# Kernel optimization log

Hardware: AMD Instinct MI355X
Metric: run time of the kernel (lower is better)

Reference implementation:

```python
import jax, jax.numpy as jnp
import numpy as np
from jax import lax

D3 = 48      # manifold_dim * 3
M = 512      # mem_slots
H = 256      # slot_dim
K = 32       # topk
IN = 1024    # input_dim
ODE_HID = 128
ODE_STEPS = 2
ODE_DT = 0.5
TEMP = 1.0   # temperature buffer
LN_EPS = 1e-5


def _ln(x, g, b):
    m = jnp.mean(x, axis=-1, keepdims=True)
    v = jnp.mean(jnp.square(x - m), axis=-1, keepdims=True)
    return (x - m) * lax.rsqrt(v + LN_EPS) * g + b


def setup_inputs() -> dict:
    key = jax.random.key(0)
    ks = jax.random.split(key, 12)
    s_in = 1.0 / np.sqrt(IN)
    s_h = 1.0 / np.sqrt(H)
    s_d3 = 1.0 / np.sqrt(D3)
    s_ode = 1.0 / np.sqrt(ODE_HID)
    return {
        "x": jax.random.normal(ks[0], (16, 2048, IN), jnp.float32),
        "w1": jax.random.uniform(ks[1], (IN, D3), jnp.float32, -s_in, s_in),
        "b1": jnp.zeros((D3,), jnp.float32),
        "g1": jnp.ones((D3,), jnp.float32),
        "be1": jnp.zeros((D3,), jnp.float32),
        "wa": jax.random.uniform(ks[2], (D3, ODE_HID), jnp.float32, -s_d3, s_d3),
        "ba": jnp.zeros((ODE_HID,), jnp.float32),
        "wb": jax.random.uniform(ks[3], (ODE_HID, D3), jnp.float32, -s_ode, s_ode),
        "bb": jnp.zeros((D3,), jnp.float32),
        "mem": jax.random.normal(ks[4], (M, H), jnp.float32),
        "pos": jax.random.normal(ks[5], (M, 16, 3), jnp.float32),
        "curv": jax.random.normal(ks[6], (M, 16), jnp.float32),
        "alpha": jnp.float32(0.1),
        "wo": jax.random.uniform(ks[7], (H, IN), jnp.float32, -s_h, s_h),
        "bo": jnp.zeros((IN,), jnp.float32),
        "go": jnp.ones((IN,), jnp.float32),
        "beo": jnp.zeros((IN,), jnp.float32),
    }


def reference(x, w1, b1, g1, be1, wa, ba, wb, bb, mem, pos, curv, alpha, wo, bo, go, beo):
    # manifold projection: Linear -> LayerNorm -> GELU, viewed as (B,S,D,3)
    h = jax.nn.gelu(_ln(x @ w1 + b1, g1, be1), approximate=False)  # (B,S,48)
    # ODE evolution (2 fixed steps over the flattened manifold coords)
    for _ in range(ODE_STEPS):
        dx = jnp.tanh(h @ wa + ba) @ wb + bb
        h = h + ODE_DT * dx
    # attend: query side is detached in the original
    q = lax.stop_gradient(h)                       # (B,S,48)
    mem_pos = pos.reshape(M, -1)                   # (512,48)
    # squared pairwise L2: ||q||^2 - 2 q.m + ||m||^2
    dist = (jnp.sum(q * q, axis=-1, keepdims=True)
            - 2.0 * jnp.einsum('bsd,md->bsm', q, mem_pos)
            + jnp.sum(mem_pos * mem_pos, axis=-1))
    dist = jnp.maximum(dist, 0.0) / max(TEMP, 1e-6)
    curv_w = jnp.exp(-alpha * jnp.linalg.norm(curv, axis=-1))  # (512,)
    dist = dist * curv_w[None, None, :]
    # topk smallest distances
    neg_top, itop = lax.top_k(-dist, K)            # (B,S,K)
    w = jax.nn.softmax(neg_top, axis=-1)           # softmax(-dtop)
    slots = mem[itop]                              # (B,S,K,256) gather
    attended = jnp.einsum('bsk,bskh->bsh', w, slots)
    # output projection: Linear -> LayerNorm -> GELU
    return jax.nn.gelu(_ln(attended @ wo + bo, go, beo), approximate=False)
```

## Files before the change

kernel.cpp:

```cpp
#include <hip/hip_runtime.h>
#include <stdint.h>

typedef unsigned short u16;
typedef __attribute__((ext_vector_type(4))) short short4v;
typedef __attribute__((ext_vector_type(8))) short short8v;
typedef __attribute__((ext_vector_type(4))) float f32x4;
typedef __attribute__((address_space(1))) void gv;
typedef __attribute__((address_space(3))) void lv;

#define NTOK 32768

__device__ __forceinline__ float bf2f(u16 u){ return __uint_as_float(((uint32_t)u)<<16); }
__device__ __forceinline__ u16 f2bf(float f){
  uint32_t u = __float_as_uint(f);
  u += 0x7FFFu + ((u>>16)&1u);
  return (u16)(u>>16);
}
__device__ __forceinline__ void hilo(float v, u16& h, u16& l){
  h = f2bf(v);
  l = f2bf(v - bf2f(h));
}
__device__ __forceinline__ void tsplit(float v, u16& h, u16& l){
  uint32_t b = __float_as_uint(v);
  h = (u16)(b >> 16);
  float lf = v - __uint_as_float(b & 0xFFFF0000u);
  l = (u16)(__float_as_uint(lf) >> 16);
}
__device__ __forceinline__ void tpack8(float4 a, float4 b, short8v& hi, short8v& lo){
  float v[8] = {a.x,a.y,a.z,a.w,b.x,b.y,b.z,b.w};
  #pragma unroll
  for (int i=0;i<8;++i){ u16 h,l; tsplit(v[i],h,l); hi[i]=(short)h; lo[i]=(short)l; }
}
__device__ __forceinline__ float fexp2(float x){ float r; asm("v_exp_f32 %0, %1" : "=v"(r) : "v"(x)); return r; }
__device__ __forceinline__ float frcp(float x){ float r; asm("v_rcp_f32 %0, %1" : "=v"(r) : "v"(x)); return r; }

__device__ __forceinline__ float gelu_f(float v){ return 0.5f*v*(1.0f + erff(v*0.70710678118654752440f)); }
__device__ __forceinline__ float gelu_t(float x){
  float p = x*(2.3022141f + 0.1029435f*x*x);
  float e = fexp2(p);
  float r = frcp(e + 1.0f);
  return x*(1.0f - r);
}
__device__ __forceinline__ float tanh_f(float x){
  float e = fexp2(2.8853901f*x);
  float r = frcp(e + 1.0f);
  return 1.0f - 2.0f*r;
}

__global__ __launch_bounds__(256) void k_prep(
    const float* __restrict__ w1, const float* __restrict__ wa, const float* __restrict__ wb,
    const float* __restrict__ pos, const float* __restrict__ curv,
    const float* __restrict__ mem, const float* __restrict__ wo,
    const float* __restrict__ alpha,
    u16* __restrict__ w1s, u16* __restrict__ wah, u16* __restrict__ wbh,
    float2* __restrict__ mnw,
    u16* __restrict__ memb, u16* __restrict__ woB, u16* __restrict__ posB)
{
  int i = blockIdx.x*256 + threadIdx.x;
  if (i < 49152){ int n = i>>10, k = i&1023; u16 h,l; hilo(w1[k*48+n], h, l);
                  w1s[i] = h; w1s[49152+i] = l; return; }
  i -= 49152;
  if (i < 8192){ int u = i>>6, d = i&63; float v = (d<48) ? wa[d*128+u] : 0.f;
                 u16 h,l; hilo(v,h,l); wah[i] = h; wah[8192+i] = l; return; }
  i -= 8192;
  if (i < 6144){ int n = i>>7, u = i&127; u16 h,l; hilo(wb[u*48+n], h, l);
                 wbh[i] = h; wbh[6144+i] = l; return; }
  i -= 6144;
  if (i < 512){
    float s = 0.f;
    #pragma unroll
    for (int d=0; d<48; ++d){ float v = pos[i*48+d]; s += v*v; }
    float c2 = 0.f;
    #pragma unroll
    for (int d=0; d<16; ++d){ float v = curv[i*16+d]; c2 += v*v; }
    mnw[i] = make_float2(s, expf(-alpha[0]*sqrtf(c2)));
    return;
  }
  i -= 512;
  if (i < 131072){ memb[i] = f2bf(mem[i]); return; }
  i -= 131072;
  if (i < 262144){
    int e = i & 7, ln = (i>>3)&63, n = (i>>9)&15, cpq = (i>>13)&3, kt = i>>15;
    int col = cpq*256 + n*16 + (ln & 15);
    int k   = kt*32 + (ln >> 4)*8 + e;
    woB[i] = f2bf(wo[k*1024 + col]);
    return;
  }
  i -= 262144;
  if (i < 32768){
    int e = i & 7, ln = (i>>3)&63, n = (i>>9)&31, ks = i>>14;
    int slot = n*16 + (ln&15);
    int d = ks*32 + (ln>>4)*8 + e;
    float v = (d < 48) ? pos[slot*48 + d] : 0.f;
    u16 h,l; hilo(v,h,l);
    posB[i] = h; posB[32768+i] = l;
  }
}

__global__ __launch_bounds__(256, 2) void k_proj_ode(
    const float* __restrict__ x, const u16* __restrict__ w1s,
    const float* __restrict__ b1, const float* __restrict__ g1, const float* __restrict__ be1,
    const u16* __restrict__ wah, const u16* __restrict__ wbh,
    const float* __restrict__ ba, const float* __restrict__ bb,
    float* __restrict__ hout, float* __restrict__ q2b)
{
  extern __shared__ char dynp[];
  float* xsl = (float*)dynp;
  u16*   bsl = (u16*)(dynp + 49152);
  u16* t_hi = (u16*)dynp;
  u16* t_lo = (u16*)(dynp + 16384);
  u16* h_hi = (u16*)(dynp + 32768);
  u16* h_lo = (u16*)(dynp + 40960);

  const int tid = threadIdx.x;
  const int lane = tid & 63, w = tid >> 6;
  const int l15 = lane & 15, l4 = lane >> 4;
  const int bm = blockIdx.x;
  const int arow = w*16 + l15;
  const int kb = bm & 15;

  f32x4 acc[3];
  #pragma unroll
  for (int n=0; n<3; ++n) acc[n] = (f32x4){0.f,0.f,0.f,0.f};

  auto stage_x = [&](float* dst, int kt){
    #pragma unroll
    for (int j=0; j<4; ++j){
      int idx = (j*4 + w)*64 + lane;
      int row = idx >> 4, q = idx & 15;
      int chunk = q >> 1, half = q & 1;
      const float* src = x + (size_t)(bm*64 + row)*1024 + kt*64 + ((chunk ^ (row & 7))*8 + half*4);
      __builtin_amdgcn_global_load_lds((gv*)src, (lv*)(dst + (j*4 + w)*256), 16, 0, 0);
    }
  };
  auto stage_b = [&](u16* dst, int kt){
    #pragma unroll
    for (int j=0; j<3; ++j){
      int idx = (j*4 + w)*64 + lane;
      int hl = (idx >= 384) ? 1 : 0;
      int rr = idx - hl*384;
      int row = rr >> 3, ch = rr & 7;
      const u16* src = w1s + hl*49152 + (size_t)row*1024 + kt*64 + ((ch ^ (row & 7))*8);
      __builtin_amdgcn_global_load_lds((gv*)src, (lv*)(dst + (j*4 + w)*512), 16, 0, 0);
    }
  };
  auto mfma_from = [&](const float* xb, const u16* bb){
    #pragma unroll
    for (int kq=0; kq<2; ++kq){
      int chunk = kq*4 + l4;
      int phys = chunk ^ (arow & 7);
      const float* xa = xb + arow*64 + phys*8;
      float4 a0 = *(const float4*)xa;
      float4 a1 = *(const float4*)(xa + 4);
      short8v ah, al; tpack8(a0, a1, ah, al);
      #pragma unroll
      for (int n=0; n<3; ++n){
        int brow = n*16 + l15;
        int bcx = chunk ^ (brow & 7);
        short8v bh = *(const short8v*)(bb + brow*64 + bcx*8);
        short8v bl = *(const short8v*)(bb + 3072 + brow*64 + bcx*8);
        acc[n] = __builtin_amdgcn_mfma_f32_16x16x32_bf16(ah, bh, acc[n], 0, 0, 0);
        acc[n] = __builtin_amdgcn_mfma_f32_16x16x32_bf16(ah, bl, acc[n], 0, 0, 0);
        acc[n] = __builtin_amdgcn_mfma_f32_16x16x32_bf16(al, bh, acc[n], 0, 0, 0);
      }
    }
  };

  float* x0 = xsl;         float* x1 = xsl + 4096;  float* x2 = xsl + 8192;
  u16*   b0 = bsl;         u16*   b1b = bsl + 6144;

  stage_b(b0, kb);
  stage_x(x0, kb);
  stage_x(x1, (kb + 1) & 15);

  float* xc = x0; float* xn = x1; float* xn2 = x2;
  u16* bc = b0;  u16* bn = b1b;

  for (int kt = 0; kt < 15; ++kt){
    asm volatile("s_waitcnt vmcnt(4)" ::: "memory");
    __builtin_amdgcn_s_barrier();
    __builtin_amdgcn_sched_barrier(0);
    mfma_from(xc, bc);
    stage_b(bn, (kt + 1 + kb) & 15);
    if (kt < 14) stage_x(xn2, (kt + 2 + kb) & 15);
    { float* t = xc; xc = xn; xn = xn2; xn2 = t; }
    { u16* t = bc; bc = bn; bn = t; }
  }
  asm volatile("s_waitcnt vmcnt(0)" ::: "memory");
  __builtin_amdgcn_s_barrier();
  __builtin_amdgcn_sched_barrier(0);
  mfma_from(xc, bc);

  float hreg[3][4];
  {
    float b1r[3], g1r[3], e1r[3];
    #pragma unroll
    for (int n=0; n<3; ++n){ int c = n*16 + l15; b1r[n] = b1[c]; g1r[n] = g1[c]; e1r[n] = be1[c]; }
    #pragma unroll
    for (int r=0; r<4; ++r){
      float a0 = acc[0][r] + b1r[0];
      float a1 = acc[1][r] + b1r[1];
      float a2 = acc[2][r] + b1r[2];
      float s1 = a0+a1+a2;
      float s2 = a0*a0 + a1*a1 + a2*a2;
      #pragma unroll
      for (int m=1; m<16; m<<=1){ s1 += __shfl_xor(s1, m); s2 += __shfl_xor(s2, m); }
      float mean = s1 * (1.f/48.f);
      float var  = s2 * (1.f/48.f) - mean*mean;
      float rs = rsqrtf(var + 1e-5f);
      hreg[0][r] = gelu_f((a0-mean)*rs*g1r[0] + e1r[0]);
      hreg[1][r] = gelu_f((a1-mean)*rs*g1r[1] + e1r[1]);
      hreg[2][r] = gelu_f((a2-mean)*rs*g1r[2] + e1r[2]);
    }
  }

  if (l4 < 2){
    int row = w*16 + l15;
    int ch = 6 + l4;
    int off = row*64 + (ch ^ (row & 7))*8;
    uint4 z = {0u,0u,0u,0u};
    *(uint4*)&h_hi[off] = z;
    *(uint4*)&h_lo[off] = z;
  }
  #pragma unroll
  for (int n=0; n<3; ++n)
    #pragma unroll
    for (int r=0; r<4; ++r){
      u16 hh, hl2; tsplit(hreg[n][r], hh, hl2);
      int row = w*16 + l4*4 + r;
      int col = n*16 + l15;
      int off = row*64 + ((col>>3) ^ (row & 7))*8 + (col & 7);
      h_hi[off] = hh; h_lo[off] = hl2;
    }

  float ba_r[8], bb_r[3];
  #pragma unroll
  for (int n=0; n<8; ++n) ba_r[n] = ba[n*16 + l15];
  #pragma unroll
  for (int n=0; n<3; ++n) bb_r[n] = bb[n*16 + l15];

  for (int s=0; s<2; ++s){
    f32x4 at[8];
    #pragma unroll
    for (int n=0; n<8; ++n) at[n] = (f32x4){0.f,0.f,0.f,0.f};
    #pragma unroll
    for (int kq=0; kq<2; ++kq){
      int ac = (kq*4 + l4) ^ (arow & 7);
      short8v ah = *(const short8v*)&h_hi[arow*64 + ac*8];
      short8v al = *(const short8v*)&h_lo[arow*64 + ac*8];
      #pragma unroll
      for (int n=0; n<8; ++n){
        const u16* bp = wah + (n*16 + l15)*64 + kq*32 + l4*8;
        short8v bh = *(const short8v*)bp;
        short8v bl = *(const short8v*)(bp + 8192);
        at[n] = __builtin_amdgcn_mfma_f32_16x16x32_bf16(ah, bh, at[n], 0, 0, 0);
        at[n] = __builtin_amdgcn_mfma_f32_16x16x32_bf16(ah, bl, at[n], 0, 0, 0);
        at[n] = __builtin_amdgcn_mfma_f32_16x16x32_bf16(al, bh, at[n], 0, 0, 0);
      }
    }
    #pragma unroll
    for (int n=0; n<8; ++n)
      #pragma unroll
      for (int r=0; r<4; ++r){
        float tv = tanh_f(at[n][r] + ba_r[n]);
        u16 th, tl; tsplit(tv, th, tl);
        int row = w*16 + l4*4 + r;
        int col = n*16 + l15;
        int c = col >> 3;
        int phys = (c & 8) | ((c & 7) ^ (row & 7));
        int off = row*128 + phys*8 + (col & 7);
        t_hi[off] = th; t_lo[off] = tl;
      }
    f32x4 ad[3];
    #pragma unroll
    for (int n=0; n<3; ++n) ad[n] = (f32x4){0.f,0.f,0.f,0.f};
    #pragma unroll
    for (int kq=0; kq<4; ++kq){
      int c = kq*4 + l4;
      int phys = (c & 8) | ((c & 7) ^ (arow & 7));
      short8v ah = *(const short8v*)&t_hi[arow*128 + phys*8];
      short8v al = *(const short8v*)&t_lo[arow*128 + phys*8];
      #pragma unroll
      for (int n=0; n<3; ++n){
        const u16* bp = wbh + (n*16 + l15)*128 + kq*32 + l4*8;
        short8v bh = *(const short8v*)bp;
        short8v bl = *(const short8v*)(bp + 6144);
        ad[n] = __builtin_amdgcn_mfma_f32_16x16x32_bf16(ah, bh, ad[n], 0, 0, 0);
        ad[n] = __builtin_amdgcn_mfma_f32_16x16x32_bf16(ah, bl, ad[n], 0, 0, 0);
        ad[n] = __builtin_amdgcn_mfma_f32_16x16x32_bf16(al, bh, ad[n], 0, 0, 0);
      }
    }
    #pragma unroll
    for (int n=0; n<3; ++n)
      #pragma unroll
      for (int r=0; r<4; ++r)
        hreg[n][r] += 0.5f*(ad[n][r] + bb_r[n]);
    if (s == 0){
      #pragma unroll
      for (int n=0; n<3; ++n)
        #pragma unroll
        for (int r=0; r<4; ++r){
          u16 hh, hl2; tsplit(hreg[n][r], hh, hl2);
          int row = w*16 + l4*4 + r;
          int col = n*16 + l15;
          int off = row*64 + ((col>>3) ^ (row & 7))*8 + (col & 7);
          h_hi[off] = hh; h_lo[off] = hl2;
        }
    }
  }
  #pragma unroll
  for (int r=0; r<4; ++r){
    size_t row = (size_t)(bm*64 + w*16 + l4*4 + r);
    #pragma unroll
    for (int n=0; n<3; ++n)
      hout[row*64 + n*16 + l15] = hreg[n][r];
    hout[row*64 + 48 + l15] = 0.f;
    float s2 = hreg[0][r]*hreg[0][r] + hreg[1][r]*hreg[1][r] + hreg[2][r]*hreg[2][r];
    #pragma unroll
    for (int msk=1; msk<16; msk<<=1) s2 += __shfl_xor(s2, msk);
    if (l15 == 0) q2b[row] = s2;
  }
}

__global__ __launch_bounds__(256, 4) void k_sel(
    const float* __restrict__ h, const float* __restrict__ q2b,
    const u16* __restrict__ posB, const float2* __restrict__ mnw,
    uint32_t* __restrict__ glist)
{
  __shared__ __align__(16) uint32_t tokKeys[2*4*528];

  const int tid = threadIdx.x;
  const int lane = tid & 63, w = tid >> 6;
  const int g = w >> 1, s = w & 1;
  const int l15 = lane & 15, l4 = lane >> 4;
  const int bm = blockIdx.x;

  const float* hrow = h + (size_t)(bm*32 + g*16 + l15)*64;
  float4 x0 = *(const float4*)(hrow + l4*8);
  float4 x1 = *(const float4*)(hrow + l4*8 + 4);
  float4 x2 = *(const float4*)(hrow + 32 + l4*8);
  float4 x3 = *(const float4*)(hrow + 32 + l4*8 + 4);
  short8v ah0, al0, ah1, al1;
  tpack8(x0, x1, ah0, al0);
  tpack8(x2, x3, ah1, al1);

  float4 q2v = *(const float4*)(q2b + bm*32 + g*16 + l4*4);
  float q2a[4] = {q2v.x, q2v.y, q2v.z, q2v.w};

  uint32_t kk[16][4];
  #pragma unroll
  for (int n=0; n<16; ++n){
    const u16* pb = posB + (size_t)(s*16 + n)*512 + lane*8;
    short8v bh0 = *(const short8v*)(pb);
    short8v bl0 = *(const short8v*)(pb + 32768);
    short8v bh1 = *(const short8v*)(pb + 16384);
    short8v bl1 = *(const short8v*)(pb + 49152);
    f32x4 acc = (f32x4){0.f,0.f,0.f,0.f};
    acc = __builtin_amdgcn_mfma_f32_16x16x32_bf16(ah0, bh0, acc, 0, 0, 0);
    acc = __builtin_amdgcn_mfma_f32_16x16x32_bf16(ah0, bl0, acc, 0, 0, 0);
    acc = __builtin_amdgcn_mfma_f32_16x16x32_bf16(al0, bh0, acc, 0, 0, 0);
    acc = __builtin_amdgcn_mfma_f32_16x16x32_bf16(ah1, bh1, acc, 0, 0, 0);
    acc = __builtin_amdgcn_mfma_f32_16x16x32_bf16(ah1, bl1, acc, 0, 0, 0);
    acc = __builtin_amdgcn_mfma_f32_16x16x32_bf16(al1, bh1, acc, 0, 0, 0);
    const int slot = s*256 + n*16 + l15;
    float2 mw = mnw[slot];
    #pragma unroll
    for (int r=0; r<4; ++r){
      float dd = fmaxf(q2a[r] + mw.x - 2.f*acc[r], 0.f) * mw.y;
      kk[n][r] = (__float_as_uint(dd) & 0xFFFFFE00u) | (uint32_t)slot;
    }
  }

  const int gbase = g*2112;
  const unsigned long long ltmask = (lane == 63) ? 0x7FFFFFFFFFFFFFFFull : ((1ull << lane) - 1ull);
  #pragma unroll
  for (int r=0; r<4; ++r){
    __syncthreads();
    #pragma unroll
    for (int n=0; n<16; ++n)
      tokKeys[gbase + l4*528 + s*256 + n*16 + l15] = kk[n][r];
    __syncthreads();
    uint32_t key8[2][8];
    #pragma unroll
    for (int j=0; j<2; ++j){
      *(uint4*)&key8[j][0] = *(const uint4*)&tokKeys[gbase + (s*2+j)*528 + lane*8];
      *(uint4*)&key8[j][4] = *(const uint4*)&tokKeys[gbase + (s*2+j)*528 + lane*8 + 4];
    }
    uint32_t p[2] = {0u,0u};
    for (int b=30; b>=0; --b){
      #pragma unroll
      for (int j=0; j<2; ++j){
        uint32_t c = p[j] | (1u<<b);
        int cnt = 0;
        #pragma unroll
        for (int i=0; i<8; ++i) cnt += (int)__popcll(__ballot(key8[j][i] < c));
        if (cnt <= 31) p[j] = c;
      }
    }
    #pragma unroll
    for (int j=0; j<2; ++j){
      size_t tok = (size_t)bm*32 + g*16 + (s*2+j)*4 + r;
      int base = 0;
      #pragma unroll
      for (int i=0; i<8; ++i){
        unsigned long long bal = __ballot(key8[j][i] <= p[j]);
        if (key8[j][i] <= p[j]){
          int idx = base + (int)__popcll(bal & ltmask);
          glist[tok*32 + idx] = key8[j][i];
        }
        base += (int)__popcll(bal);
      }
    }
  }
}

__global__ __launch_bounds__(256) void k_attend(
    const uint32_t* __restrict__ glist, const u16* __restrict__ memb,
    u16* __restrict__ att)
{
  const int lane = threadIdx.x & 63, w = threadIdx.x >> 6;
  const size_t tok = (size_t)blockIdx.x*4 + w;
  uint32_t lk[32];
  const uint4* lp = (const uint4*)(glist + tok*32);
  #pragma unroll
  for (int q=0; q<8; ++q) *(uint4*)&lk[q*4] = lp[q];
  uint32_t km = lk[0];
  #pragma unroll
  for (int i=1; i<32; ++i) km = min(km, lk[i]);
  const float dminf = __uint_as_float(km & 0xFFFFFE00u);

  float den = 0.f, a0=0.f, a1=0.f, a2=0.f, a3=0.f;
  #pragma unroll
  for (int i=0; i<32; ++i){
    float dk = __uint_as_float(lk[i] & 0xFFFFFE00u);
    int slot = (int)(lk[i] & 511u);
    float wg = __expf(dminf - dk);
    den += wg;
    uint2 mv = ((const uint2*)(memb + (size_t)slot*256))[lane];
    a0 += wg*bf2f((u16)(mv.x & 0xFFFFu));
    a1 += wg*bf2f((u16)(mv.x >> 16));
    a2 += wg*bf2f((u16)(mv.y & 0xFFFFu));
    a3 += wg*bf2f((u16)(mv.y >> 16));
  }
  float inv = frcp(den);
  uint32_t o0 = (uint32_t)f2bf(a0*inv) | ((uint32_t)f2bf(a1*inv) << 16);
  uint32_t o1 = (uint32_t)f2bf(a2*inv) | ((uint32_t)f2bf(a3*inv) << 16);
  ((uint2*)(att + tok*256))[lane] = make_uint2(o0, o1);
}

__global__ __launch_bounds__(1024, 4) void k_out(
    const u16* __restrict__ A, const u16* __restrict__ woB, const float* __restrict__ bo,
    const float* __restrict__ go, const float* __restrict__ beo, float* __restrict__ out)
{
  __shared__ u16 Asl[64*256];
  __shared__ float redS1[64][65];
  __shared__ float redS2[64][65];
  __shared__ float finM[64], finR[64];

  const int tid = threadIdx.x;
  const int lane = tid & 63, w = tid >> 6;
  const int l15 = lane & 15, l4 = lane >> 4;
  const int bm = blockIdx.x;

  #pragma unroll
  for (int j=0; j<2; ++j){
    int idx = j*1024 + tid;
    int row = idx >> 5, ch = idx & 31;
    int gc = (ch & 24) | ((ch & 7) ^ (row & 7));
    uint4 v = *(const uint4*)(A + (size_t)(bm*64 + row)*256 + gc*8);
    *(uint4*)&Asl[row*256 + ch*8] = v;
  }
  __syncthreads();

  f32x4 acc[4][4];
  #pragma unroll
  for (int m=0; m<4; ++m)
    #pragma unroll
    for (int n=0; n<4; ++n) acc[m][n] = (f32x4){0.f,0.f,0.f,0.f};

  #pragma unroll
  for (int kt=0; kt<8; ++kt){
    const int c = kt*4 + l4;
    short8v af[4];
    #pragma unroll
    for (int m=0; m<4; ++m){
      int arow = m*16 + l15;
      int aphys = (c & 24) | ((c & 7) ^ (arow & 7));
      af[m] = *(const short8v*)&Asl[arow*256 + aphys*8];
    }
    const u16* bbase = woB + ((size_t)kt*64 + w*4)*512 + lane*8;
    #pragma unroll
    for (int n=0; n<4; ++n){
      short8v bf = *(const short8v*)(bbase + n*512);
      #pragma unroll
      for (int m=0; m<4; ++m)
        acc[m][n] = __builtin_amdgcn_mfma_f32_16x16x32_bf16(af[m], bf, acc[m][n], 0, 0, 0);
    }
  }

  float bor[4];
  #pragma unroll
  for (int n=0; n<4; ++n) bor[n] = bo[w*64 + n*16 + l15];

  float s1[4][4], s2[4][4];
  #pragma unroll
  for (int m=0; m<4; ++m)
    #pragma unroll
    for (int r=0; r<4; ++r){ s1[m][r] = 0.f; s2[m][r] = 0.f; }
  #pragma unroll
  for (int m=0; m<4; ++m)
    #pragma unroll
    for (int n=0; n<4; ++n)
      #pragma unroll
      for (int r=0; r<4; ++r){
        float v = acc[m][n][r] + bor[n];
        acc[m][n][r] = v;
        s1[m][r] += v; s2[m][r] += v*v;
      }
  #pragma unroll
  for (int m=0; m<4; ++m)
    #pragma unroll
    for (int r=0; r<4; ++r){
      s1[m][r] += __shfl_xor(s1[m][r], 1);
      s2[m][r] += __shfl_xor(s2[m][r], 1);
      s1[m][r] += __shfl_xor(s1[m][r], 2);
      s2[m][r] += __shfl_xor(s2[m][r], 2);
    }
  if ((l15 & 3) == 0){
    int q = l15 >> 2;
    #pragma unroll
    for (int m=0; m<4; ++m)
      #pragma unroll
      for (int r=0; r<4; ++r){
        int row = m*16 + l4*4 + r;
        redS1[row][w*4 + q] = s1[m][r];
        redS2[row][w*4 + q] = s2[m][r];
      }
  }
  __syncthreads();

  {
    int row = w*4 + (lane >> 4);
    int p0 = lane & 15;
    float a1 = redS1[row][p0] + redS1[row][p0+16] + redS1[row][p0+32] + redS1[row][p0+48];
    float a2 = redS2[row][p0] + redS2[row][p0+16] + redS2[row][p0+32] + redS2[row][p0+48];
    #pragma unroll
    for (int msk=1; msk<16; msk<<=1){
      a1 += __shfl_xor(a1, msk);
      a2 += __shfl_xor(a2, msk);
    }
    if (p0 == 0){
      float mu = a1 * (1.f/1024.f);
      float var = a2 * (1.f/1024.f) - mu*mu;
      finM[row] = mu;
      finR[row] = rsqrtf(var + 1e-5f);
    }
  }
  __syncthreads();

  float4 muv[4], rsv[4];
  #pragma unroll
  for (int m=0; m<4; ++m){
    muv[m] = *(const float4*)&finM[m*16 + l4*4];
    rsv[m] = *(const float4*)&finR[m*16 + l4*4];
  }

  float gor[4], eor[4];
  #pragma unroll
  for (int n=0; n<4; ++n){
    int col = w*64 + n*16 + l15;
    gor[n] = go[col]; eor[n] = beo[col];
  }
  #pragma unroll
  for (int m=0; m<4; ++m)
    #pragma unroll
    for (int r=0; r<4; ++r){
      size_t row = (size_t)bm*64 + m*16 + l4*4 + r;
      float* op = out + row*1024 + w*64 + l15;
      float mu = ((const float*)&muv[m])[r];
      float rv = ((const float*)&rsv[m])[r];
      #pragma unroll
      for (int n=0; n<4; ++n){
        op[n*16] = gelu_t((acc[m][n][r] - mu)*rv*gor[n] + eor[n]);
      }
    }
}

extern "C" void kernel_launch(void* const* d_in, const int* in_sizes, int n_in,
                              void* d_out, int out_size, void* d_ws, size_t ws_size,
                              hipStream_t stream) {
  const float* x    = (const float*)d_in[0];
  const float* w1   = (const float*)d_in[1];
  const float* b1   = (const float*)d_in[2];
  const float* g1   = (const float*)d_in[3];
  const float* be1  = (const float*)d_in[4];
  const float* wa   = (const float*)d_in[5];
  const float* ba   = (const float*)d_in[6];
  const float* wb   = (const float*)d_in[7];
  const float* bb   = (const float*)d_in[8];
  const float* mem  = (const float*)d_in[9];
  const float* pos  = (const float*)d_in[10];
  const float* curv = (const float*)d_in[11];
  const float* alpha= (const float*)d_in[12];
  const float* wo   = (const float*)d_in[13];
  const float* bo   = (const float*)d_in[14];
  const float* go   = (const float*)d_in[15];
  const float* beo  = (const float*)d_in[16];
  float* out = (float*)d_out;

  char* ws = (char*)d_ws;
  size_t o = 0;
  auto take = [&](size_t b) -> char* { char* p = ws + o; o += (b + 255) & ~(size_t)255; return p; };
  char*  regA   = take(67108864);
  float* hbuf64 = (float*)(regA + 6291456);
  float* q2b    = (float*)(regA + 6291456 + 8388608);
  u16*   att    = (u16*)take(16777216);
  u16*   w1s    = (u16*)take(196608);
  u16*   wah    = (u16*)take(32768);
  u16*   wbh    = (u16*)take(24576);
  float2* mnw   = (float2*)take(4096);
  u16*   memb   = (u16*)take(262144);
  u16*   woB    = (u16*)take(524288);
  u16*   posB   = (u16*)take(131072);
  uint32_t* glist = (uint32_t*)take(4194304);

  hipFuncSetAttribute((const void*)k_proj_ode, hipFuncAttributeMaxDynamicSharedMemorySize, 73728);

  k_prep<<<1914, 256, 0, stream>>>(w1, wa, wb, pos, curv, mem, wo, alpha,
                                   w1s, wah, wbh, mnw, memb, woB, posB);
  k_proj_ode<<<512, 256, 73728, stream>>>(x, w1s, b1, g1, be1, wah, wbh, ba, bb,
                                          hbuf64, q2b);
  k_sel<<<1024, 256, 0, stream>>>(hbuf64, q2b, posB, mnw, glist);
  k_attend<<<8192, 256, 0, stream>>>(glist, memb, att);
  k_out<<<512, 1024, 0, stream>>>(att, woB, bo, go, beo, out);
  (void)in_sizes; (void)n_in; (void)out_size; (void)ws_size;
}
```

Measured before the change: 237.3 us.

## Load W1 fragments directly into registers and deepen x LDS pipeline to four stages

```diff
diff --git a/kernel.cpp b/kernel.cpp
--- a/kernel.cpp
+++ b/kernel.cpp
@@ -106,7 +106,6 @@
 {
   extern __shared__ char dynp[];
   float* xsl = (float*)dynp;
-  u16*   bsl = (u16*)(dynp + 49152);
   u16* t_hi = (u16*)dynp;
   u16* t_lo = (u16*)(dynp + 16384);
   u16* h_hi = (u16*)(dynp + 32768);
@@ -133,18 +132,17 @@
       __builtin_amdgcn_global_load_lds((gv*)src, (lv*)(dst + (j*4 + w)*256), 16, 0, 0);
     }
   };
-  auto stage_b = [&](u16* dst, int kt){
-    #pragma unroll
-    for (int j=0; j<3; ++j){
-      int idx = (j*4 + w)*64 + lane;
-      int hl = (idx >= 384) ? 1 : 0;
-      int rr = idx - hl*384;
-      int row = rr >> 3, ch = rr & 7;
-      const u16* src = w1s + hl*49152 + (size_t)row*1024 + kt*64 + ((ch ^ (row & 7))*8);
-      __builtin_amdgcn_global_load_lds((gv*)src, (lv*)(dst + (j*4 + w)*512), 16, 0, 0);
-    }
+  auto loadB = [&](int ktabs, short8v* Bh, short8v* Bl){
+    #pragma unroll
+    for (int kq=0; kq<2; ++kq)
+      #pragma unroll
+      for (int n=0; n<3; ++n){
+        const u16* bp = w1s + (size_t)(n*16 + l15)*1024 + ktabs*64 + kq*32 + l4*8;
+        Bh[kq*3+n] = *(const short8v*)bp;
+        Bl[kq*3+n] = *(const short8v*)(bp + 49152);
+      }
   };
-  auto mfma_from = [&](const float* xb, const u16* bb){
+  auto mfma_from = [&](const float* xb, const short8v* Bh, const short8v* Bl){
     #pragma unroll
     for (int kq=0; kq<2; ++kq){
       int chunk = kq*4 + l4;
@@ -155,41 +153,39 @@
       short8v ah, al; tpack8(a0, a1, ah, al);
       #pragma unroll
       for (int n=0; n<3; ++n){
-        int brow = n*16 + l15;
-        int bcx = chunk ^ (brow & 7);
-        short8v bh = *(const short8v*)(bb + brow*64 + bcx*8);
-        short8v bl = *(const short8v*)(bb + 3072 + brow*64 + bcx*8);
-        acc[n] = __builtin_amdgcn_mfma_f32_16x16x32_bf16(ah, bh, acc[n], 0, 0, 0);
-        acc[n] = __builtin_amdgcn_mfma_f32_16x16x32_bf16(ah, bl, acc[n], 0, 0, 0);
-        acc[n] = __builtin_amdgcn_mfma_f32_16x16x32_bf16(al, bh, acc[n], 0, 0, 0);
+        acc[n] = __builtin_amdgcn_mfma_f32_16x16x32_bf16(ah, Bh[kq*3+n], acc[n], 0, 0, 0);
+        acc[n] = __builtin_amdgcn_mfma_f32_16x16x32_bf16(ah, Bl[kq*3+n], acc[n], 0, 0, 0);
+        acc[n] = __builtin_amdgcn_mfma_f32_16x16x32_bf16(al, Bh[kq*3+n], acc[n], 0, 0, 0);
       }
     }
   };
 
-  float* x0 = xsl;         float* x1 = xsl + 4096;  float* x2 = xsl + 8192;
-  u16*   b0 = bsl;         u16*   b1b = bsl + 6144;
-
-  stage_b(b0, kb);
-  stage_x(x0, kb);
-  stage_x(x1, (kb + 1) & 15);
-
-  float* xc = x0; float* xn = x1; float* xn2 = x2;
-  u16* bc = b0;  u16* bn = b1b;
-
-  for (int kt = 0; kt < 15; ++kt){
-    asm volatile("s_waitcnt vmcnt(4)" ::: "memory");
+  short8v Bh0[6], Bl0[6], Bh1[6], Bl1[6];
+
+  stage_x(xsl,         kb);
+  stage_x(xsl + 4096,  (kb + 1) & 15);
+  stage_x(xsl + 8192,  (kb + 2) & 15);
+  loadB(kb, Bh0, Bl0);
+
+  #pragma unroll
+  for (int kt = 0; kt < 16; ++kt){
+    if      (kt == 0)  asm volatile("s_waitcnt vmcnt(20)" ::: "memory");
+    else if (kt == 1)  asm volatile("s_waitcnt vmcnt(32)" ::: "memory");
+    else if (kt == 2)  asm volatile("s_waitcnt vmcnt(44)" ::: "memory");
+    else if (kt <= 13) asm volatile("s_waitcnt vmcnt(32)" ::: "memory");
+    else if (kt == 14) asm volatile("s_waitcnt vmcnt(28)" ::: "memory");
+    else               asm volatile("s_waitcnt vmcnt(24)" ::: "memory");
     __builtin_amdgcn_s_barrier();
     __builtin_amdgcn_sched_barrier(0);
-    mfma_from(xc, bc);
-    stage_b(bn, (kt + 1 + kb) & 15);
-    if (kt < 14) stage_x(xn2, (kt + 2 + kb) & 15);
-    { float* t = xc; xc = xn; xn = xn2; xn2 = t; }
-    { u16* t = bc; bc = bn; bn = t; }
-  }
-  asm volatile("s_waitcnt vmcnt(0)" ::: "memory");
-  __builtin_amdgcn_s_barrier();
-  __builtin_amdgcn_sched_barrier(0);
-  mfma_from(xc, bc);
+    if ((kt & 1) == 0){
+      if (kt < 15) loadB((kt + 1 + kb) & 15, Bh1, Bl1);
+      mfma_from(xsl + (kt & 3)*4096, Bh0, Bl0);
+    } else {
+      if (kt < 15) loadB((kt + 1 + kb) & 15, Bh0, Bl0);
+      mfma_from(xsl + (kt & 3)*4096, Bh1, Bl1);
+    }
+    if (kt < 13) stage_x(xsl + ((kt + 3) & 3)*4096, (kt + 3 + kb) & 15);
+  }
 
   float hreg[3][4];
   {
@@ -624,11 +620,11 @@
   u16*   posB   = (u16*)take(131072);
   uint32_t* glist = (uint32_t*)take(4194304);
 
-  hipFuncSetAttribute((const void*)k_proj_ode, hipFuncAttributeMaxDynamicSharedMemorySize, 73728);
+  hipFuncSetAttribute((const void*)k_proj_ode, hipFuncAttributeMaxDynamicSharedMemorySize, 65536);
 
   k_prep<<<1914, 256, 0, stream>>>(w1, wa, wb, pos, curv, mem, wo, alpha,
                                    w1s, wah, wbh, mnw, memb, woB, posB);
-  k_proj_ode<<<512, 256, 73728, stream>>>(x, w1s, b1, g1, be1, wah, wbh, ba, bb,
+  k_proj_ode<<<512, 256, 65536, stream>>>(x, w1s, b1, g1, be1, wah, wbh, ba, bb,
                                           hbuf64, q2b);
   k_sel<<<1024, 256, 0, stream>>>(hbuf64, q2b, posB, mnw, glist);
   k_attend<<<8192, 256, 0, stream>>>(glist, memb, att);
```

New measurement: 250.3 us. 1.05x slower.
